# Kernel optimization log

Hardware: AMD Instinct MI355X
Metric: run time of the kernel (lower is better)

Reference implementation:

```python
import jax, jax.numpy as jnp
import numpy as np
from jax import lax
jax.config.update('jax_enable_x64', True)

SR = 44100
BLOCK = 512
N_MELS = 80
N_ALLPASS = 256
N_HARM = 512
N_NOISE = 256
HID = 256
B = 16
NF = 400
T = NF * BLOCK
N_OUT = N_ALLPASS + N_HARM + N_NOISE


def upsample(sig, factor):
    # torch: interpolate(cat(sig, sig[-1:]), size=n*factor+1, mode='linear', align_corners=True)[:-1]
    b, n, c = sig.shape
    ext = jnp.concatenate([sig, sig[:, -1:]], axis=1)  # (b, n+1, c)
    w = (jnp.arange(factor, dtype=jnp.float32) / factor)[None, None, :, None]
    up = ext[:, :-1, None, :] * (1.0 - w) + ext[:, 1:, None, :] * w
    return up.reshape(b, n * factor, c)


def hann_periodic(n):
    return 0.5 - 0.5 * jnp.cos(2.0 * np.pi * jnp.arange(n, dtype=jnp.float32) / n)


def freq_impulse_response(mag, hann_window, half_width=None):
    # mag: (b, nf, m) complex -> ir: (b, nf, 2*(m-1)) in causal (rolled) form
    ir = jnp.fft.irfft(mag).astype(jnp.float32)
    n = ir.shape[-1]
    if hann_window:
        if half_width is None:
            w = jnp.roll(hann_periodic(n), n // 2)
            ir = jnp.roll(ir * w, n // 2, axis=-1)
        else:
            # dynamic hann window with per-frame half width (b, nf, 1)
            w = jnp.arange(-(n // 2), (n + 1) // 2, dtype=jnp.float32) / half_width
            w = jnp.where(w > 1.0, 0.0, w)
            w = (1.0 + jnp.cos(np.pi * w)) * 0.5
            ir = jnp.roll(ir, n // 2, axis=-1) * w
    else:
        ir = jnp.roll(ir, n // 2, axis=-1)
    return ir


def fft_convolve(audio, ir):
    b, t = audio.shape
    nf, ir_size = ir.shape[1], ir.shape[2]
    hop = t // nf
    frame = 2 * hop
    fft_size = frame + ir_size - 1
    chunks = jnp.pad(audio, ((0, 0), (hop, hop))).reshape(b, nf + 2, hop)
    frames = jnp.concatenate([chunks[:, :-1], chunks[:, 1:]], axis=-1)  # (b, nf+1, frame)
    bart = 1.0 - jnp.abs(2.0 * jnp.arange(frame, dtype=jnp.float32) / frame - 1.0)
    frames = frames * bart
    ir_ext = jnp.concatenate([ir, ir[:, -1:]], axis=1)  # repeat last IR frame
    out_f = jnp.fft.irfft(jnp.fft.rfft(frames, fft_size) * jnp.fft.rfft(ir_ext, fft_size), fft_size).astype(jnp.float32)
    n_out = nf + 1
    length = (n_out - 1) * hop + fft_size
    idx = (jnp.arange(n_out)[:, None] * hop + jnp.arange(fft_size)[None, :]).reshape(-1)
    out = jnp.zeros((b, length), jnp.float32).at[:, idx].add(out_f.reshape(b, -1))
    return out[:, hop:t + hop]


def conv1d_same(x, w, bias):
    y = lax.conv_general_dilated(x, w, (1,), [(1, 1)], dimension_numbers=('NCH', 'OIH', 'NCH'))
    return y + bias[None, :, None]


def mel2ctrl(mel, phase, conv1_w, conv1_b, gn_g, gn_b, conv2_w, conv2_b, phase_w, phase_b, ln_g, ln_b, out_w, out_b):
    h = conv1d_same(mel.transpose(0, 2, 1), conv1_w, conv1_b)  # (b, 256, nf)
    b, c, l = h.shape
    g = h.reshape(b, 4, c // 4, l)  # GroupNorm(4, 256)
    mu = g.mean((2, 3), keepdims=True)
    var = g.var((2, 3), keepdims=True)
    h = ((g - mu) / jnp.sqrt(var + 1e-5)).reshape(b, c, l)
    h = h * gn_g[None, :, None] + gn_b[None, :, None]
    h = jnp.where(h >= 0, h, 0.01 * h)  # LeakyReLU
    h = conv1d_same(h, conv2_w, conv2_b).transpose(0, 2, 1)  # (b, nf, 256)
    pe = jnp.concatenate([jnp.sin(phase), jnp.cos(phase)], axis=-1) @ phase_w.T + phase_b
    h = h + pe
    mu = h.mean(-1, keepdims=True)
    var = h.var(-1, keepdims=True)
    h = (h - mu) / jnp.sqrt(var + 1e-5) * ln_g + ln_b
    out = h @ out_w.T + out_b
    gd = out[..., :N_ALLPASS]
    hm = out[..., N_ALLPASS:N_ALLPASS + N_HARM]
    nm = out[..., N_ALLPASS + N_HARM:]
    return gd, hm, nm


def setup_inputs():
    key = jax.random.key(0)
    ks = jax.random.split(key, 8)
    s = 0.02
    return {
        'mel_frames': jax.random.normal(ks[0], (B, NF, N_MELS), jnp.float32),
        'f0_frames': jax.random.uniform(ks[1], (B, NF, 1), jnp.float32) * 400.0 + 100.0,
        'initial_phase': jnp.zeros((B, 1, 1), jnp.float32),
        'uniform_noise': jax.random.uniform(ks[2], (B, T), jnp.float32),
        'conv1_w': jax.random.normal(ks[3], (HID, N_MELS, 3), jnp.float32) * s,
        'conv1_b': jnp.zeros((HID,), jnp.float32),
        'gn_g': jnp.ones((HID,), jnp.float32),
        'gn_b': jnp.zeros((HID,), jnp.float32),
        'conv2_w': jax.random.normal(ks[4], (HID, HID, 3), jnp.float32) * s,
        'conv2_b': jnp.zeros((HID,), jnp.float32),
        'phase_w': jax.random.normal(ks[5], (HID, 2), jnp.float32) * s,
        'phase_b': jnp.zeros((HID,), jnp.float32),
        'ln_g': jnp.ones((HID,), jnp.float32),
        'ln_b': jnp.zeros((HID,), jnp.float32),
        'out_w': jax.random.normal(ks[6], (N_OUT, HID), jnp.float32) * s,
        'out_b': jnp.zeros((N_OUT,), jnp.float32),
    }


def reference(mel_frames, f0_frames, initial_phase, uniform_noise, conv1_w, conv1_b, gn_g, gn_b, conv2_w, conv2_b, phase_w, phase_b, ln_g, ln_b, out_w, out_b):
    f0 = upsample(f0_frames, BLOCK)  # (B, T, 1)
    # double-precision wrapped phase accumulation
    x = jnp.cumsum(f0.astype(jnp.float64) / SR, axis=1) + initial_phase.astype(jnp.float64) / (2.0 * np.pi)
    x = (x - jnp.round(x)).astype(jnp.float32)
    phase_frames = 2.0 * np.pi * x[:, ::BLOCK, :]  # (B, NF, 1)
    gd_raw, hm_raw, nm_raw = mel2ctrl(mel_frames, phase_frames, conv1_w, conv1_b, gn_g, gn_b, conv2_w, conv2_b, phase_w, phase_b, ln_g, ln_b, out_w, out_b)
    group_delay = np.pi * jnp.tanh(gd_raw)
    src_param = jnp.exp(hm_raw)
    noise_param = jnp.exp(nm_raw) / 128.0
    combtooth = jnp.sinc(SR * x / (f0 + 0.001))[..., 0]  # (B, T)
    allpass = jnp.exp(1j * jnp.cumsum(group_delay, axis=-1).astype(jnp.complex64))
    harmonic = fft_convolve(combtooth, freq_impulse_response(allpass, hann_window=False))
    half_width = 1.5 * SR / (f0_frames + 0.001)  # (B, NF, 1)
    harmonic = fft_convolve(harmonic, freq_impulse_response(src_param.astype(jnp.complex64), True, half_width))
    noise = uniform_noise * 2.0 - 1.0
    noise = fft_convolve(noise, freq_impulse_response(noise_param.astype(jnp.complex64), True, None))
    signal = harmonic + noise
    return signal, phase_frames, harmonic, noise
```

## Files before the change

### kernel.cpp

```cpp
#include <hip/hip_runtime.h>
#include <math.h>

#define BATCH 16
#define NF_ 400
#define TLEN 204800
#define NMELS 80
#define HID 256
#define SRD 44100.0

static constexpr size_t S_ = 1638400;
static constexpr size_t OFF_COMB = 0;
static constexpr size_t OFF_H1   = 2 * S_;
static constexpr size_t OFF_H2   = 3 * S_;
static constexpr size_t OFF_IR1  = 2 * S_;
static constexpr size_t OFF_PHI  = 4 * S_;
static constexpr size_t OFF_NSP  = 5 * S_;
static constexpr size_t OFF_HTMP = 4 * S_;
static constexpr size_t OFF_SRC  = 6 * S_;
static constexpr size_t OFF_IR3  = 6 * S_;
static constexpr size_t OFF_IR2  = 8 * S_;
static constexpr size_t OFF_FSUM = 12 * S_;
static constexpr size_t OFF_PREF = 12 * S_ + 12800;
static constexpr size_t OFF_GN   = 12 * S_ + 25600;

__device__ __forceinline__ float cs7_f0_at(const float* f0f, int b, int n, int k) {
    float a = f0f[b * NF_ + n];
    float c = f0f[b * NF_ + min(n + 1, NF_ - 1)];
    float w = (float)k * (1.0f / 512.0f);
    return __fadd_rn(__fmul_rn(a, 1.0f - w), __fmul_rn(c, w));
}

__global__ void cs7_fsum(const float* __restrict__ f0f, double* __restrict__ fsum) {
    int gid = blockIdx.x * blockDim.x + threadIdx.x;
    if (gid >= BATCH * NF_) return;
    int b = gid / NF_, n = gid % NF_;
    double s = 0.0;
    for (int k = 0; k < 512; ++k) s += (double)cs7_f0_at(f0f, b, n, k) / SRD;
    fsum[gid] = s;
}

__global__ void cs7_prefix(const double* __restrict__ fsum, double* __restrict__ pref) {
    int b = threadIdx.x;
    if (b >= BATCH) return;
    double run = 0.0;
    for (int n = 0; n < NF_; ++n) { pref[b * NF_ + n] = run; run += fsum[b * NF_ + n]; }
}

__global__ __launch_bounds__(512) void cs7_phase(const float* __restrict__ f0f,
        const float* __restrict__ ip, const double* __restrict__ pref,
        float* __restrict__ comb, float* __restrict__ phase_out) {
    __shared__ double sc[512];
    int b = blockIdx.x / NF_, n = blockIdx.x % NF_;
    int k = threadIdx.x;
    float f0 = cs7_f0_at(f0f, b, n, k);
    sc[k] = (double)f0 / SRD;
    __syncthreads();
    for (int off = 1; off < 512; off <<= 1) {
        double v = (k >= off) ? sc[k - off] : 0.0;
        __syncthreads();
        sc[k] += v;
        __syncthreads();
    }
    double xd = pref[b * NF_ + n] + sc[k] + (double)ip[b] / (2.0 * M_PI);
    xd -= rint(xd);
    float xf = (float)xd;
    double zd = 44100.0 * (double)xf / ((double)f0 + 0.001);
    double pz = M_PI * zd;
    comb[(size_t)b * TLEN + n * 512 + k] = (zd == 0.0) ? 1.0f : (float)(sin(pz) / pz);
    if (k == 0) phase_out[b * NF_ + n] = (float)(2.0 * M_PI * (double)xf);
}

__global__ __launch_bounds__(256) void cs7_conv1x3(const float* __restrict__ mel,
        const float* __restrict__ w1, const float* __restrict__ b1, float* __restrict__ h1) {
    __shared__ float m3[3][NMELS];
    int b = blockIdx.x / NF_, l = blockIdx.x % NF_;
    int tid = threadIdx.x;
    for (int i = tid; i < 3 * NMELS; i += 256) {
        int tap = i / NMELS, ic = i % NMELS;
        int li = l + tap - 1;
        m3[tap][ic] = (li >= 0 && li < NF_) ? mel[((size_t)b * NF_ + li) * NMELS + ic] : 0.0f;
    }
    __syncthreads();
    int oc = tid;
    double acc = (double)b1[oc];
    const float* wp = w1 + (size_t)oc * NMELS * 3;
    for (int ic = 0; ic < NMELS; ++ic)
        acc += (double)m3[0][ic] * (double)wp[ic * 3]
             + (double)m3[1][ic] * (double)wp[ic * 3 + 1]
             + (double)m3[2][ic] * (double)wp[ic * 3 + 2];
    h1[((size_t)b * NF_ + l) * HID + oc] = (float)acc;
}

__global__ __launch_bounds__(256) void cs7_gnstats(const float* __restrict__ h1, float* __restrict__ gn) {
    __shared__ double rs[256], rq[256];
    int b = blockIdx.x >> 2, g = blockIdx.x & 3;
    int tid = threadIdx.x;
    double s = 0.0, q = 0.0;
    for (int i = tid; i < 64 * NF_; i += 256) {
        int l = i >> 6, c = g * 64 + (i & 63);
        float v = h1[((size_t)b * NF_ + l) * HID + c];
        s += v; q += (double)v * v;
    }
    rs[tid] = s; rq[tid] = q;
    __syncthreads();
    for (int off = 128; off > 0; off >>= 1) {
        if (tid < off) { rs[tid] += rs[tid + off]; rq[tid] += rq[tid + off]; }
        __syncthreads();
    }
    if (tid == 0) {
        double mu = rs[0] / (64.0 * NF_);
        double var = rq[0] / (64.0 * NF_) - mu * mu;
        gn[blockIdx.x * 2] = (float)mu;
        gn[blockIdx.x * 2 + 1] = (float)(1.0 / sqrt(var + 1e-5));
    }
}

__global__ __launch_bounds__(256) void cs7_conv2ln(const float* __restrict__ h1,
        const float* __restrict__ gn, const float* __restrict__ gng, const float* __restrict__ gnb,
        const float* __restrict__ w2, const float* __restrict__ b2,
        const float* __restrict__ pw, const float* __restrict__ pb,
        const float* __restrict__ lng, const float* __restrict__ lnb,
        const float* __restrict__ phase, float* __restrict__ h2) {
    __shared__ float cols[10][HID];
    __shared__ double rsum[256], rsq[256];
    int b = blockIdx.x / 50, l0 = (blockIdx.x % 50) * 8;
    int tid = threadIdx.x;
    for (int i = tid; i < 10 * HID; i += 256) {
        int lc = i >> 8, c = i & 255;
        int l = l0 + lc - 1;
        float v = 0.0f;
        if (l >= 0 && l < NF_) {
            float hv = h1[((size_t)b * NF_ + l) * HID + c];
            int g = c >> 6;
            double vv = ((double)hv - (double)gn[(b * 4 + g) * 2]) * (double)gn[(b * 4 + g) * 2 + 1]
                        * (double)gng[c] + (double)gnb[c];
            v = (float)(vv >= 0.0 ? vv : 0.01 * vv);
        }
        cols[lc][c] = v;
    }
    __syncthreads();
    int oc = tid;
    double acc[8];
    #pragma unroll
    for (int lt = 0; lt < 8; ++lt) acc[lt] = (double)b2[oc];
    const float* wp = w2 + (size_t)oc * HID * 3;
    for (int ic = 0; ic < HID; ++ic) {
        double w0 = (double)wp[ic * 3], w1v = (double)wp[ic * 3 + 1], w2v = (double)wp[ic * 3 + 2];
        float cc[10];
        #pragma unroll
        for (int j = 0; j < 10; ++j) cc[j] = cols[j][ic];
        #pragma unroll
        for (int lt = 0; lt < 8; ++lt)
            acc[lt] += (double)cc[lt] * w0 + (double)cc[lt + 1] * w1v + (double)cc[lt + 2] * w2v;
    }
    for (int lt = 0; lt < 8; ++lt) {
        int l = l0 + lt;
        double ph = (double)phase[b * NF_ + l];
        double sp, cp; sincos(ph, &sp, &cp);
        double v = acc[lt] + sp * (double)pw[oc * 2] + cp * (double)pw[oc * 2 + 1] + (double)pb[oc];
        rsum[tid] = v; rsq[tid] = v * v;
        __syncthreads();
        for (int off = 128; off > 0; off >>= 1) {
            if (tid < off) { rsum[tid] += rsum[tid + off]; rsq[tid] += rsq[tid + off]; }
            __syncthreads();
        }
        double mu = rsum[0] * (1.0 / 256.0);
        double var = rsq[0] * (1.0 / 256.0) - mu * mu;
        double rstd = 1.0 / sqrt(var + 1e-5);
        __syncthreads();
        h2[((size_t)b * NF_ + l) * HID + oc] = (float)((v - mu) * rstd * (double)lng[oc] + (double)lnb[oc]);
    }
}

__global__ __launch_bounds__(256) void cs7_proj(const float* __restrict__ h2,
        const float* __restrict__ ow, const float* __restrict__ ob,
        float* __restrict__ phi, float* __restrict__ srcspec, float* __restrict__ nspec) {
    __shared__ float hrow[8][HID];
    __shared__ double ssc[256];
    int b = blockIdx.x / 50, l0 = (blockIdx.x % 50) * 8;
    int tid = threadIdx.x;
    for (int i = tid; i < 8 * HID; i += 256) {
        int lc = i >> 8, c = i & 255;
        hrow[lc][c] = h2[((size_t)b * NF_ + l0 + lc) * HID + c];
    }
    __syncthreads();
    double a0[8], a1[8], a2[8], a3[8];
    #pragma unroll
    for (int lt = 0; lt < 8; ++lt) {
        a0[lt] = (double)ob[tid];       a1[lt] = (double)ob[256 + tid];
        a2[lt] = (double)ob[512 + tid]; a3[lt] = (double)ob[768 + tid];
    }
    const float* w0p = ow + (size_t)tid * HID;
    const float* w1p = ow + (size_t)(256 + tid) * HID;
    const float* w2p = ow + (size_t)(512 + tid) * HID;
    const float* w3p = ow + (size_t)(768 + tid) * HID;
    for (int ic = 0; ic < HID; ++ic) {
        double w0 = (double)w0p[ic], w1v = (double)w1p[ic], w2v = (double)w2p[ic], w3v = (double)w3p[ic];
        #pragma unroll
        for (int lt = 0; lt < 8; ++lt) {
            double h = (double)hrow[lt][ic];
            a0[lt] += h * w0; a1[lt] += h * w1v; a2[lt] += h * w2v; a3[lt] += h * w3v;
        }
    }
    for (int lt = 0; lt < 8; ++lt) {
        size_t bl = (size_t)b * NF_ + (l0 + lt);
        double gdv = M_PI * tanh(a0[lt]);
        ssc[tid] = gdv;
        __syncthreads();
        for (int off = 1; off < 256; off <<= 1) {
            double v = (tid >= off) ? ssc[tid - off] : 0.0;
            __syncthreads();
            ssc[tid] += v;
            __syncthreads();
        }
        phi[bl * 256 + tid] = (float)ssc[tid];
        __syncthreads();
        srcspec[bl * 512 + tid] = (float)exp(a1[lt]);
        srcspec[bl * 512 + 256 + tid] = (float)exp(a2[lt]);
        nspec[bl * 256 + tid] = (float)(exp(a3[lt]) * (1.0 / 128.0));
    }
}

__global__ __launch_bounds__(256) void cs7_ir_allpass(const float* __restrict__ phi, float* __restrict__ ir1) {
    __shared__ float cph[256], sph[256];
    size_t bl = blockIdx.x;
    int tid = threadIdx.x;
    {
        float ph = phi[bl * 256 + tid];
        cph[tid] = 2.0f * cosf(ph); sph[tid] = 2.0f * sinf(ph);
    }
    __syncthreads();
    for (int t = tid; t < 510; t += 256) {
        double ang = 2.0 * M_PI * (double)t / 510.0;
        double srd_, crd; sincos(ang, &srd_, &crd);
        double sj, cj;    sincos(16.0 * ang, &sj, &cj);
        float crf = (float)crd, srf = (float)srd_;
        double cD = crd, sD = srd_;
        float acc = 0.5f * (cph[0] + ((t & 1) ? -cph[255] : cph[255]));
        for (int k0 = 1; k0 <= 254; k0 += 16) {
            float c = (float)cD, s = (float)sD;
            int ke = min(k0 + 16, 255);
            for (int k = k0; k < ke; ++k) {
                acc += cph[k] * c - sph[k] * s;
                float cn = c * crf - s * srf;
                float sn = s * crf + c * srf;
                c = cn; s = sn;
            }
            double nc = cD * cj - sD * sj;
            double ns = sD * cj + cD * sj;
            cD = nc; sD = ns;
        }
        int j = t + 255; if (j >= 510) j -= 510;
        ir1[bl * 510 + j] = acc * (1.0f / 510.0f);
    }
}

__device__ __forceinline__ float cs7_hw_win(int j, float hw) {
    float wv = (float)(j - 511) / hw;
    if (wv > 1.0f) wv = 0.0f;
    return (1.0f + cosf((float)M_PI * wv)) * 0.5f;
}

__global__ __launch_bounds__(256) void cs7_ir_src(const float* __restrict__ srcspec,
        const float* __restrict__ f0f, float* __restrict__ ir2) {
    __shared__ float sp[512];
    size_t bl = blockIdx.x;
    int b = blockIdx.x / NF_, l = blockIdx.x % NF_;
    int tid = threadIdx.x;
    sp[tid] = 2.0f * srcspec[bl * 512 + tid];
    sp[tid + 256] = 2.0f * srcspec[bl * 512 + 256 + tid];
    __syncthreads();
    float hw = 66150.0f / (f0f[b * NF_ + l] + 0.001f);
    for (int t = tid; t < 512; t += 256) {
        double ang = 2.0 * M_PI * (double)t / 1022.0;
        double srd_, crd; sincos(ang, &srd_, &crd);
        double sj, cj;    sincos(16.0 * ang, &sj, &cj);
        float crf = (float)crd, srf = (float)srd_;
        double cD = crd, sD = srd_;
        float acc = 0.5f * (sp[0] + ((t & 1) ? -sp[511] : sp[511]));
        for (int k0 = 1; k0 <= 510; k0 += 16) {
            float c = (float)cD, s = (float)sD;
            int ke = min(k0 + 16, 511);
            for (int k = k0; k < ke; ++k) {
                acc += sp[k] * c;
                float cn = c * crf - s * srf;
                float sn = s * crf + c * srf;
                c = cn; s = sn;
            }
            double nc = cD * cj - sD * sj;
            double ns = sD * cj + cD * sj;
            cD = nc; sD = ns;
        }
        float raw = acc * (1.0f / 1022.0f);
        {
            int j = t + 511; if (j >= 1022) j -= 1022;
            ir2[bl * 1022 + j] = raw * cs7_hw_win(j, hw);
        }
        if (t >= 1 && t <= 510) {
            int j = 511 - t;
            ir2[bl * 1022 + j] = raw * cs7_hw_win(j, hw);
        }
    }
}

__global__ __launch_bounds__(256) void cs7_ir_noise(const float* __restrict__ nspec, float* __restrict__ ir3) {
    __shared__ float sp[256];
    size_t bl = blockIdx.x;
    int t = threadIdx.x;
    sp[t] = 2.0f * nspec[bl * 256 + t];
    __syncthreads();
    double ang = 2.0 * M_PI * (double)t / 510.0;
    double srd_, crd; sincos(ang, &srd_, &crd);
    double sj, cj;    sincos(16.0 * ang, &sj, &cj);
    float crf = (float)crd, srf = (float)srd_;
    double cD = crd, sD = srd_;
    float acc = 0.5f * (sp[0] + ((t & 1) ? -sp[255] : sp[255]));
    for (int k0 = 1; k0 <= 254; k0 += 16) {
        float c = (float)cD, s = (float)sD;
        int ke = min(k0 + 16, 255);
        for (int k = k0; k < ke; ++k) {
            acc += sp[k] * c;
            float cn = c * crf - s * srf;
            float sn = s * crf + c * srf;
            c = cn; s = sn;
        }
        double nc = cD * cj - sD * sj;
        double ns = sD * cj + cD * sj;
        cD = nc; sD = ns;
    }
    float raw = acc * (1.0f / 510.0f);
    {
        int j = t + 255; if (j >= 510) j -= 510;
        float win = 0.5f - 0.5f * cosf((float)(2.0 * M_PI) * (float)j / 510.0f);
        ir3[bl * 510 + j] = raw * win;
    }
    if (t >= 1 && t <= 254) {
        int j = 255 - t;
        float win = 0.5f - 0.5f * cosf((float)(2.0 * M_PI) * (float)j / 510.0f);
        ir3[bl * 510 + j] = raw * win;
    }
}

template<int IRS, int NFRM, int MOFF>
__global__ __launch_bounds__(256) void cs7_conv(const float* __restrict__ audio,
        const float* __restrict__ ir, float* __restrict__ out, float scale, float shift) {
    constexpr int PAD = 264;
    constexpr int W   = (IRS + 2 * PAD + 3) & ~3;
    constexpr int FRW = 1040;
    __shared__ float4 sir4[NFRM][W / 4];
    __shared__ float4 fr4[NFRM][FRW / 4];
    float* sir = (float*)sir4;
    float* frp = (float*)fr4;
    int b = blockIdx.x / 200, q = blockIdx.x % 200;
    int t0 = q * 1024;
    int m_lo = 2 * q + MOFF;
    int tid = threadIdx.x;

    for (int i = tid; i < NFRM * FRW; i += 256) {
        int fi = i / FRW, kk = i - fi * FRW;
        int k = kk - 6;
        float sv = 0.0f;
        if (k >= 0 && k < 1024) {
            int m = m_lo + fi;
            int idx = (m << 9) + k - 512;
            float v = 0.0f;
            if (m >= 0 && m <= 400 && idx >= 0 && idx < TLEN)
                v = audio[(size_t)b * TLEN + idx] * scale + shift;
            float bart = 1.0f - fabsf((float)k * (1.0f / 512.0f) - 1.0f);
            sv = v * bart;
        }
        frp[fi * FRW + kk] = sv;
    }
    for (int i = tid; i < NFRM * W; i += 256) {
        int fi = i / W, x = i - fi * W;
        int j = (IRS - 1 + PAD) - x;
        int m = m_lo + fi;
        float v = 0.0f;
        if (j >= 0 && j < IRS && m >= 0 && m <= 400)
            v = ir[((size_t)b * NF_ + min(m, 399)) * IRS + j];
        sir[fi * W + x] = v;
    }
    __syncthreads();

    int tb = t0 + tid * 4;
    int wtid0 = tid & ~63;
    float acc0 = 0, acc1 = 0, acc2 = 0, acc3 = 0;
    #pragma unroll
    for (int fi = 0; fi < NFRM; ++fi) {
        int m = m_lo + fi;
        if (m < 0 || m > 400) continue;
        int d0w = t0 + wtid0 * 4 + 512 - (m << 9);
        int klo = max(0, d0w - (IRS - 1));
        int khi = min(1023, d0w + 255);
        if (klo > khi) continue;
        int kc0 = (((klo - 2) & ~3) + 2);
        int nch = ((khi - kc0) >> 2) + 1;
        int d0  = t0 + tid * 4 + 512 - (m << 9);
        const float4* sp = (const float4*)(sir + fi * W + ((IRS + PAD - 4) - d0 + kc0));
        const float4* fp = (const float4*)(frp + fi * FRW + 6 + kc0);
        float4 A = sp[0];
        for (int c = 0; c < nch; ++c) {
            float4 B = sp[c + 1];
            float4 F = fp[c];
            acc3 += F.x * A.x; acc2 += F.x * A.y; acc1 += F.x * A.z; acc0 += F.x * A.w;
            acc3 += F.y * A.y; acc2 += F.y * A.z; acc1 += F.y * A.w; acc0 += F.y * B.x;
            acc3 += F.z * A.z; acc2 += F.z * A.w; acc1 += F.z * B.x; acc0 += F.z * B.y;
            acc3 += F.w * A.w; acc2 += F.w * B.x; acc1 += F.w * B.y; acc0 += F.w * B.z;
            A = B;
        }
    }
    *(float4*)(out + (size_t)b * TLEN + tb) = make_float4(acc0, acc1, acc2, acc3);
}

__global__ void cs7_add(const float* __restrict__ a, const float* __restrict__ b,
                        float* __restrict__ o, int n4) {
    int i = blockIdx.x * blockDim.x + threadIdx.x;
    if (i < n4) {
        float4 x = ((const float4*)a)[i];
        float4 y = ((const float4*)b)[i];
        ((float4*)o)[i] = make_float4(x.x + y.x, x.y + y.y, x.z + y.z, x.w + y.w);
    }
}

extern "C" void kernel_launch(void* const* d_in, const int* in_sizes, int n_in,
                              void* d_out, int out_size, void* d_ws, size_t ws_size,
                              hipStream_t stream) {
    const float* mel   = (const float*)d_in[0];
    const float* f0f   = (const float*)d_in[1];
    const float* ip    = (const float*)d_in[2];
    const float* unoi  = (const float*)d_in[3];
    const float* w1    = (const float*)d_in[4];
    const float* b1    = (const float*)d_in[5];
    const float* gng   = (const float*)d_in[6];
    const float* gnb   = (const float*)d_in[7];
    const float* w2    = (const float*)d_in[8];
    const float* b2    = (const float*)d_in[9];
    const float* pw    = (const float*)d_in[10];
    const float* pb    = (const float*)d_in[11];
    const float* lng   = (const float*)d_in[12];
    const float* lnb   = (const float*)d_in[13];
    const float* ow    = (const float*)d_in[14];
    const float* ob    = (const float*)d_in[15];
    float* out = (float*)d_out;
    float* ws  = (float*)d_ws;

    float*  comb = ws + OFF_COMB;
    float*  h1   = ws + OFF_H1;
    float*  h2   = ws + OFF_H2;
    float*  ir1  = ws + OFF_IR1;
    float*  phi  = ws + OFF_PHI;
    float*  nsp  = ws + OFF_NSP;
    float*  htmp = ws + OFF_HTMP;
    float*  ssp  = ws + OFF_SRC;
    float*  ir3  = ws + OFF_IR3;
    float*  ir2  = ws + OFF_IR2;
    double* fsum = (double*)(ws + OFF_FSUM);
    double* pref = (double*)(ws + OFF_PREF);
    float*  gn   = ws + OFF_GN;

    float* out_sig   = out;
    float* out_phase = out + (size_t)BATCH * TLEN;
    float* out_harm  = out_phase + BATCH * NF_;
    float* out_noise = out_harm + (size_t)BATCH * TLEN;

    cs7_fsum<<<25, 256, 0, stream>>>(f0f, fsum);
    cs7_prefix<<<1, 16, 0, stream>>>(fsum, pref);
    cs7_phase<<<BATCH * NF_, 512, 0, stream>>>(f0f, ip, pref, comb, out_phase);
    cs7_conv1x3<<<BATCH * NF_, 256, 0, stream>>>(mel, w1, b1, h1);
    cs7_gnstats<<<64, 256, 0, stream>>>(h1, gn);
    cs7_conv2ln<<<BATCH * 50, 256, 0, stream>>>(h1, gn, gng, gnb, w2, b2, pw, pb, lng, lnb, out_phase, h2);
    cs7_proj<<<BATCH * 50, 256, 0, stream>>>(h2, ow, ob, phi, ssp, nsp);
    cs7_ir_allpass<<<BATCH * NF_, 256, 0, stream>>>(phi, ir1);
    cs7_ir_src<<<BATCH * NF_, 256, 0, stream>>>(ssp, f0f, ir2);
    cs7_ir_noise<<<BATCH * NF_, 256, 0, stream>>>(nsp, ir3);
    cs7_conv<510, 4, -1><<<BATCH * 200, 256, 0, stream>>>(comb, ir1, htmp, 1.0f, 0.0f);
    cs7_conv<1022, 5, -2><<<BATCH * 200, 256, 0, stream>>>(htmp, ir2, out_harm, 1.0f, 0.0f);
    cs7_conv<510, 4, -1><<<BATCH * 200, 256, 0, stream>>>(unoi, ir3, out_noise, 2.0f, -1.0f);
    cs7_add<<<(BATCH * TLEN / 4 + 255) / 256, 256, 0, stream>>>(out_harm, out_noise, out_sig, BATCH * TLEN / 4);
}
```

Baseline: 2.853 ms.

## Pre-window frames in global memory and widen direct-conv tiles to 8 outputs per thread

Producers now write Bartlett-windowed overlapping frames straight into a frame buffer. The phase kernel and the first harmonic convolution each write their output split into two crossfade halves, and a staging kernel does the same for noise. The convolution kernel reads those frames from global memory instead of rebuilding them in LDS. Each thread now computes 8 outputs instead of 4 over a 2048-sample tile, using a swizzled LDS IR row and a 3-way unrolled register rotation, which cuts LDS traffic per FMA. This costs extra memsets, a staging pass, more workspace and per-thread registers, and frames are re-read from global/L2 instead of shared memory.

```diff
diff --git a/kernel.cpp b/kernel.cpp
--- a/kernel.cpp
+++ b/kernel.cpp
@@ -8,51 +8,47 @@
 #define HID 256
 #define SRD 44100.0
 
-static constexpr size_t S_ = 1638400;
-static constexpr size_t OFF_COMB = 0;
-static constexpr size_t OFF_H1   = 2 * S_;
-static constexpr size_t OFF_H2   = 3 * S_;
-static constexpr size_t OFF_IR1  = 2 * S_;
-static constexpr size_t OFF_PHI  = 4 * S_;
-static constexpr size_t OFF_NSP  = 5 * S_;
-static constexpr size_t OFF_HTMP = 4 * S_;
-static constexpr size_t OFF_SRC  = 6 * S_;
-static constexpr size_t OFF_IR3  = 6 * S_;
-static constexpr size_t OFF_IR2  = 8 * S_;
-static constexpr size_t OFF_FSUM = 12 * S_;
-static constexpr size_t OFF_PREF = 12 * S_ + 12800;
-static constexpr size_t OFF_GN   = 12 * S_ + 25600;
-
-__device__ __forceinline__ float cs7_f0_at(const float* f0f, int b, int n, int k) {
+static constexpr size_t S_   = 1638400;
+static constexpr size_t FRSZ = (size_t)6416 * 1028;
+static constexpr size_t OFF_A    = 0;
+static constexpr size_t OFF_JN   = FRSZ;
+static constexpr size_t OFF_SSP  = 2 * FRSZ;
+static constexpr size_t OFF_IR1  = OFF_SSP + 2 * S_;
+static constexpr size_t OFF_IR3  = OFF_IR1 + 3264000;
+static constexpr size_t OFF_FSUM = OFF_IR3 + 3264000;
+static constexpr size_t OFF_PREF = OFF_FSUM + 12800;
+static constexpr size_t OFF_GN   = OFF_PREF + 12800;
+
+__device__ __forceinline__ float cs8_f0_at(const float* f0f, int b, int n, int k) {
     float a = f0f[b * NF_ + n];
     float c = f0f[b * NF_ + min(n + 1, NF_ - 1)];
     float w = (float)k * (1.0f / 512.0f);
     return __fadd_rn(__fmul_rn(a, 1.0f - w), __fmul_rn(c, w));
 }
 
-__global__ void cs7_fsum(const float* __restrict__ f0f, double* __restrict__ fsum) {
+__global__ void cs8_fsum(const float* __restrict__ f0f, double* __restrict__ fsum) {
     int gid = blockIdx.x * blockDim.x + threadIdx.x;
     if (gid >= BATCH * NF_) return;
     int b = gid / NF_, n = gid % NF_;
     double s = 0.0;
-    for (int k = 0; k < 512; ++k) s += (double)cs7_f0_at(f0f, b, n, k) / SRD;
+    for (int k = 0; k < 512; ++k) s += (double)cs8_f0_at(f0f, b, n, k) / SRD;
     fsum[gid] = s;
 }
 
-__global__ void cs7_prefix(const double* __restrict__ fsum, double* __restrict__ pref) {
+__global__ void cs8_prefix(const double* __restrict__ fsum, double* __restrict__ pref) {
     int b = threadIdx.x;
     if (b >= BATCH) return;
     double run = 0.0;
     for (int n = 0; n < NF_; ++n) { pref[b * NF_ + n] = run; run += fsum[b * NF_ + n]; }
 }
 
-__global__ __launch_bounds__(512) void cs7_phase(const float* __restrict__ f0f,
+__global__ __launch_bounds__(512) void cs8_phase(const float* __restrict__ f0f,
         const float* __restrict__ ip, const double* __restrict__ pref,
-        float* __restrict__ comb, float* __restrict__ phase_out) {
+        float* __restrict__ frA, float* __restrict__ phase_out) {
     __shared__ double sc[512];
     int b = blockIdx.x / NF_, n = blockIdx.x % NF_;
     int k = threadIdx.x;
-    float f0 = cs7_f0_at(f0f, b, n, k);
+    float f0 = cs8_f0_at(f0f, b, n, k);
     sc[k] = (double)f0 / SRD;
     __syncthreads();
     for (int off = 1; off < 512; off <<= 1) {
@@ -66,11 +62,15 @@
     float xf = (float)xd;
     double zd = 44100.0 * (double)xf / ((double)f0 + 0.001);
     double pz = M_PI * zd;
-    comb[(size_t)b * TLEN + n * 512 + k] = (zd == 0.0) ? 1.0f : (float)(sin(pz) / pz);
+    float cv = (zd == 0.0) ? 1.0f : (float)(sin(pz) / pz);
+    float wb = (float)k * (1.0f / 512.0f);
+    size_t row = (size_t)(b * 401 + n) * 1028;
+    frA[row + 512 + k]  = cv * (1.0f - wb);
+    frA[row + 1028 + k] = cv * wb;
     if (k == 0) phase_out[b * NF_ + n] = (float)(2.0 * M_PI * (double)xf);
 }
 
-__global__ __launch_bounds__(256) void cs7_conv1x3(const float* __restrict__ mel,
+__global__ __launch_bounds__(256) void cs8_conv1x3(const float* __restrict__ mel,
         const float* __restrict__ w1, const float* __restrict__ b1, float* __restrict__ h1) {
     __shared__ float m3[3][NMELS];
     int b = blockIdx.x / NF_, l = blockIdx.x % NF_;
@@ -91,7 +91,7 @@
     h1[((size_t)b * NF_ + l) * HID + oc] = (float)acc;
 }
 
-__global__ __launch_bounds__(256) void cs7_gnstats(const float* __restrict__ h1, float* __restrict__ gn) {
+__global__ __launch_bounds__(256) void cs8_gnstats(const float* __restrict__ h1, float* __restrict__ gn) {
     __shared__ double rs[256], rq[256];
     int b = blockIdx.x >> 2, g = blockIdx.x & 3;
     int tid = threadIdx.x;
@@ -115,7 +115,7 @@
     }
 }
 
-__global__ __launch_bounds__(256) void cs7_conv2ln(const float* __restrict__ h1,
+__global__ __launch_bounds__(256) void cs8_conv2ln(const float* __restrict__ h1,
         const float* __restrict__ gn, const float* __restrict__ gng, const float* __restrict__ gnb,
         const float* __restrict__ w2, const float* __restrict__ b2,
         const float* __restrict__ pw, const float* __restrict__ pb,
@@ -172,7 +172,7 @@
     }
 }
 
-__global__ __launch_bounds__(256) void cs7_proj(const float* __restrict__ h2,
+__global__ __launch_bounds__(256) void cs8_proj(const float* __restrict__ h2,
         const float* __restrict__ ow, const float* __restrict__ ob,
         float* __restrict__ phi, float* __restrict__ srcspec, float* __restrict__ nspec) {
     __shared__ float hrow[8][HID];
@@ -221,7 +221,7 @@
     }
 }
 
-__global__ __launch_bounds__(256) void cs7_ir_allpass(const float* __restrict__ phi, float* __restrict__ ir1) {
+__global__ __launch_bounds__(256) void cs8_ir_allpass(const float* __restrict__ phi, float* __restrict__ ir1) {
     __shared__ float cph[256], sph[256];
     size_t bl = blockIdx.x;
     int tid = threadIdx.x;
@@ -255,13 +255,13 @@
     }
 }
 
-__device__ __forceinline__ float cs7_hw_win(int j, float hw) {
+__device__ __forceinline__ float cs8_hw_win(int j, float hw) {
     float wv = (float)(j - 511) / hw;
     if (wv > 1.0f) wv = 0.0f;
     return (1.0f + cosf((float)M_PI * wv)) * 0.5f;
 }
 
-__global__ __launch_bounds__(256) void cs7_ir_src(const float* __restrict__ srcspec,
+__global__ __launch_bounds__(256) void cs8_ir_src(const float* __restrict__ srcspec,
         const float* __restrict__ f0f, float* __restrict__ ir2) {
     __shared__ float sp[512];
     size_t bl = blockIdx.x;
@@ -294,16 +294,16 @@
         float raw = acc * (1.0f / 1022.0f);
         {
             int j = t + 511; if (j >= 1022) j -= 1022;
-            ir2[bl * 1022 + j] = raw * cs7_hw_win(j, hw);
+            ir2[bl * 1022 + j] = raw * cs8_hw_win(j, hw);
         }
         if (t >= 1 && t <= 510) {
             int j = 511 - t;
-            ir2[bl * 1022 + j] = raw * cs7_hw_win(j, hw);
-        }
-    }
-}
-
-__global__ __launch_bounds__(256) void cs7_ir_noise(const float* __restrict__ nspec, float* __restrict__ ir3) {
+            ir2[bl * 1022 + j] = raw * cs8_hw_win(j, hw);
+        }
+    }
+}
+
+__global__ __launch_bounds__(256) void cs8_ir_noise(const float* __restrict__ nspec, float* __restrict__ ir3) {
     __shared__ float sp[256];
     size_t bl = blockIdx.x;
     int t = threadIdx.x;
@@ -341,78 +341,120 @@
     }
 }
 
-template<int IRS, int NFRM, int MOFF>
-__global__ __launch_bounds__(256) void cs7_conv(const float* __restrict__ audio,
-        const float* __restrict__ ir, float* __restrict__ out, float scale, float shift) {
-    constexpr int PAD = 264;
-    constexpr int W   = (IRS + 2 * PAD + 3) & ~3;
-    constexpr int FRW = 1040;
-    __shared__ float4 sir4[NFRM][W / 4];
-    __shared__ float4 fr4[NFRM][FRW / 4];
-    float* sir = (float*)sir4;
-    float* frp = (float*)fr4;
-    int b = blockIdx.x / 200, q = blockIdx.x % 200;
-    int t0 = q * 1024;
-    int m_lo = 2 * q + MOFF;
-    int tid = threadIdx.x;
-
-    for (int i = tid; i < NFRM * FRW; i += 256) {
-        int fi = i / FRW, kk = i - fi * FRW;
-        int k = kk - 6;
-        float sv = 0.0f;
-        if (k >= 0 && k < 1024) {
-            int m = m_lo + fi;
-            int idx = (m << 9) + k - 512;
-            float v = 0.0f;
-            if (m >= 0 && m <= 400 && idx >= 0 && idx < TLEN)
-                v = audio[(size_t)b * TLEN + idx] * scale + shift;
-            float bart = 1.0f - fabsf((float)k * (1.0f / 512.0f) - 1.0f);
-            sv = v * bart;
-        }
-        frp[fi * FRW + kk] = sv;
-    }
+__global__ __launch_bounds__(256) void cs8_stagef(const float* __restrict__ audio,
+        float* __restrict__ frw, float scale, float shift) {
+    int bm = blockIdx.x;
+    int b = bm / 401, m = bm % 401;
+    int tid = threadIdx.x;
+    for (int kk = tid; kk < 1028; kk += 256) {
+        float v = 0.0f;
+        if (kk < 1024) {
+            int idx = (m << 9) + kk - 512;
+            if (idx >= 0 && idx < TLEN) {
+                float a = audio[(size_t)b * TLEN + idx] * scale + shift;
+                float bart = 1.0f - fabsf((float)kk * (1.0f / 512.0f) - 1.0f);
+                v = a * bart;
+            }
+        }
+        frw[(size_t)bm * 1028 + kk] = v;
+    }
+}
+
+__device__ __forceinline__ int cs8_swz(int B) { return B ^ ((B >> 3) & 7); }
+
+__device__ __forceinline__ void cs8_fma8(const float4 F, const float4 A,
+        const float4 B, const float4 C, float acc[8]) {
+    const float w[12] = {A.x,A.y,A.z,A.w,B.x,B.y,B.z,B.w,C.x,C.y,C.z,C.w};
+    #pragma unroll
+    for (int a = 0; a < 8; ++a)
+        acc[a] += F.x * w[8 - a] + F.y * w[9 - a] + F.z * w[10 - a] + F.w * w[11 - a];
+}
+
+template<int IRS, int NFRM, int MOFF, int FOUT>
+__global__ __launch_bounds__(256) void cs8_conv(const float* __restrict__ frw,
+        const float* __restrict__ ir, float* __restrict__ out) {
+    constexpr int PAD = 515;
+    constexpr int R = IRS - 1 + PAD;
+    constexpr int W = (R + 526) & ~3;
+    __shared__ __align__(16) float sir[NFRM][W];
+    int b = blockIdx.x / 100, q = blockIdx.x % 100;
+    int t0 = q * 2048;
+    int m_lo = (t0 >> 9) + MOFF;
+    int tid = threadIdx.x;
+
     for (int i = tid; i < NFRM * W; i += 256) {
         int fi = i / W, x = i - fi * W;
-        int j = (IRS - 1 + PAD) - x;
+        int j = R - x;
         int m = m_lo + fi;
         float v = 0.0f;
         if (j >= 0 && j < IRS && m >= 0 && m <= 400)
             v = ir[((size_t)b * NF_ + min(m, 399)) * IRS + j];
-        sir[fi * W + x] = v;
-    }
-    __syncthreads();
-
-    int tb = t0 + tid * 4;
-    int wtid0 = tid & ~63;
-    float acc0 = 0, acc1 = 0, acc2 = 0, acc3 = 0;
+        int p = (cs8_swz(x >> 2) << 2) | (x & 3);
+        sir[fi][p] = v;
+    }
+    __syncthreads();
+
+    int tb = t0 + tid * 8;
+    int wt0 = tid & ~63;
+    float acc[8] = {0, 0, 0, 0, 0, 0, 0, 0};
     #pragma unroll
     for (int fi = 0; fi < NFRM; ++fi) {
         int m = m_lo + fi;
         if (m < 0 || m > 400) continue;
-        int d0w = t0 + wtid0 * 4 + 512 - (m << 9);
+        int d0w = t0 + wt0 * 8 + 512 - (m << 9);
         int klo = max(0, d0w - (IRS - 1));
-        int khi = min(1023, d0w + 255);
+        int khi = min(1023, d0w + 511);
         if (klo > khi) continue;
-        int kc0 = (((klo - 2) & ~3) + 2);
-        int nch = ((khi - kc0) >> 2) + 1;
-        int d0  = t0 + tid * 4 + 512 - (m << 9);
-        const float4* sp = (const float4*)(sir + fi * W + ((IRS + PAD - 4) - d0 + kc0));
-        const float4* fp = (const float4*)(frp + fi * FRW + 6 + kc0);
-        float4 A = sp[0];
-        for (int c = 0; c < nch; ++c) {
-            float4 B = sp[c + 1];
-            float4 F = fp[c];
-            acc3 += F.x * A.x; acc2 += F.x * A.y; acc1 += F.x * A.z; acc0 += F.x * A.w;
-            acc3 += F.y * A.y; acc2 += F.y * A.z; acc1 += F.y * A.w; acc0 += F.y * B.x;
-            acc3 += F.z * A.z; acc2 += F.z * A.w; acc1 += F.z * B.x; acc0 += F.z * B.y;
-            acc3 += F.w * A.w; acc2 += F.w * B.x; acc1 += F.w * B.y; acc0 += F.w * B.z;
-            A = B;
-        }
-    }
-    *(float4*)(out + (size_t)b * TLEN + tb) = make_float4(acc0, acc1, acc2, acc3);
-}
-
-__global__ void cs7_add(const float* __restrict__ a, const float* __restrict__ b,
+        int kcs = __builtin_amdgcn_readfirstlane(klo & ~3);
+        int nch = ((__builtin_amdgcn_readfirstlane(khi) - kcs) >> 2) + 1;
+        int d0 = t0 + tid * 8 + 512 - (m << 9);
+        int Bb = (R - d0 + kcs - 8) >> 2;
+        const float4* row4 = (const float4*)&sir[fi][0];
+        const float4* fp4 = (const float4*)(frw + (size_t)(b * 401 + m) * 1028 + kcs);
+        float4 r0 = row4[cs8_swz(Bb)];
+        float4 r1 = row4[cs8_swz(Bb + 1)];
+        float4 r2;
+        int c = 0;
+        for (; c + 3 <= nch; c += 3) {
+            float4 F0 = fp4[c];
+            r2 = row4[cs8_swz(Bb + c + 2)];
+            cs8_fma8(F0, r0, r1, r2, acc);
+            float4 F1 = fp4[c + 1];
+            r0 = row4[cs8_swz(Bb + c + 3)];
+            cs8_fma8(F1, r1, r2, r0, acc);
+            float4 F2 = fp4[c + 2];
+            r1 = row4[cs8_swz(Bb + c + 4)];
+            cs8_fma8(F2, r2, r0, r1, acc);
+        }
+        for (; c < nch; ++c) {
+            float4 F = fp4[c];
+            r2 = row4[cs8_swz(Bb + c + 2)];
+            cs8_fma8(F, r0, r1, r2, acc);
+            r0 = r1; r1 = r2;
+        }
+    }
+    if (FOUT == 0) {
+        float* o = out + (size_t)b * TLEN + tb;
+        *(float4*)o = make_float4(acc[0], acc[1], acc[2], acc[3]);
+        *(float4*)(o + 4) = make_float4(acc[4], acc[5], acc[6], acc[7]);
+    } else {
+        int km = tb & 511;
+        int m1 = tb >> 9;
+        float* r1p = out + (size_t)(b * 401 + m1) * 1028;
+        float bw[8];
+        #pragma unroll
+        for (int j2 = 0; j2 < 8; ++j2) bw[j2] = (float)(km + j2) * (1.0f / 512.0f);
+        *(float4*)(r1p + 512 + km) = make_float4(acc[0] * (1.f - bw[0]), acc[1] * (1.f - bw[1]),
+                                                 acc[2] * (1.f - bw[2]), acc[3] * (1.f - bw[3]));
+        *(float4*)(r1p + 512 + km + 4) = make_float4(acc[4] * (1.f - bw[4]), acc[5] * (1.f - bw[5]),
+                                                     acc[6] * (1.f - bw[6]), acc[7] * (1.f - bw[7]));
+        float* r2p = r1p + 1028;
+        *(float4*)(r2p + km) = make_float4(acc[0] * bw[0], acc[1] * bw[1], acc[2] * bw[2], acc[3] * bw[3]);
+        *(float4*)(r2p + km + 4) = make_float4(acc[4] * bw[4], acc[5] * bw[5], acc[6] * bw[6], acc[7] * bw[7]);
+    }
+}
+
+__global__ void cs8_add(const float* __restrict__ a, const float* __restrict__ b,
                         float* __restrict__ o, int n4) {
     int i = blockIdx.x * blockDim.x + threadIdx.x;
     if (i < n4) {
@@ -444,16 +486,16 @@
     float* out = (float*)d_out;
     float* ws  = (float*)d_ws;
 
-    float*  comb = ws + OFF_COMB;
-    float*  h1   = ws + OFF_H1;
-    float*  h2   = ws + OFF_H2;
+    float*  frA  = ws + OFF_A;
+    float*  frJ  = ws + OFF_JN;
+    float*  h1   = ws + OFF_JN;
+    float*  h2   = ws + OFF_JN + S_;
+    float*  phi  = ws + OFF_JN + 2 * S_;
+    float*  nsp  = ws + OFF_JN + 3 * S_;
+    float*  ssp  = ws + OFF_SSP;
     float*  ir1  = ws + OFF_IR1;
-    float*  phi  = ws + OFF_PHI;
-    float*  nsp  = ws + OFF_NSP;
-    float*  htmp = ws + OFF_HTMP;
-    float*  ssp  = ws + OFF_SRC;
     float*  ir3  = ws + OFF_IR3;
-    float*  ir2  = ws + OFF_IR2;
+    float*  ir2  = ws + OFF_A;
     double* fsum = (double*)(ws + OFF_FSUM);
     double* pref = (double*)(ws + OFF_PREF);
     float*  gn   = ws + OFF_GN;
@@ -463,18 +505,21 @@
     float* out_harm  = out_phase + BATCH * NF_;
     float* out_noise = out_harm + (size_t)BATCH * TLEN;
 
-    cs7_fsum<<<25, 256, 0, stream>>>(f0f, fsum);
-    cs7_prefix<<<1, 16, 0, stream>>>(fsum, pref);
-    cs7_phase<<<BATCH * NF_, 512, 0, stream>>>(f0f, ip, pref, comb, out_phase);
-    cs7_conv1x3<<<BATCH * NF_, 256, 0, stream>>>(mel, w1, b1, h1);
-    cs7_gnstats<<<64, 256, 0, stream>>>(h1, gn);
-    cs7_conv2ln<<<BATCH * 50, 256, 0, stream>>>(h1, gn, gng, gnb, w2, b2, pw, pb, lng, lnb, out_phase, h2);
-    cs7_proj<<<BATCH * 50, 256, 0, stream>>>(h2, ow, ob, phi, ssp, nsp);
-    cs7_ir_allpass<<<BATCH * NF_, 256, 0, stream>>>(phi, ir1);
-    cs7_ir_src<<<BATCH * NF_, 256, 0, stream>>>(ssp, f0f, ir2);
-    cs7_ir_noise<<<BATCH * NF_, 256, 0, stream>>>(nsp, ir3);
-    cs7_conv<510, 4, -1><<<BATCH * 200, 256, 0, stream>>>(comb, ir1, htmp, 1.0f, 0.0f);
-    cs7_conv<1022, 5, -2><<<BATCH * 200, 256, 0, stream>>>(htmp, ir2, out_harm, 1.0f, 0.0f);
-    cs7_conv<510, 4, -1><<<BATCH * 200, 256, 0, stream>>>(unoi, ir3, out_noise, 2.0f, -1.0f);
-    cs7_add<<<(BATCH * TLEN / 4 + 255) / 256, 256, 0, stream>>>(out_harm, out_noise, out_sig, BATCH * TLEN / 4);
-}
+    hipMemsetAsync(frA, 0, FRSZ * sizeof(float), stream);
+    cs8_fsum<<<25, 256, 0, stream>>>(f0f, fsum);
+    cs8_prefix<<<1, 16, 0, stream>>>(fsum, pref);
+    cs8_phase<<<BATCH * NF_, 512, 0, stream>>>(f0f, ip, pref, frA, out_phase);
+    cs8_conv1x3<<<BATCH * NF_, 256, 0, stream>>>(mel, w1, b1, h1);
+    cs8_gnstats<<<64, 256, 0, stream>>>(h1, gn);
+    cs8_conv2ln<<<BATCH * 50, 256, 0, stream>>>(h1, gn, gng, gnb, w2, b2, pw, pb, lng, lnb, out_phase, h2);
+    cs8_proj<<<BATCH * 50, 256, 0, stream>>>(h2, ow, ob, phi, ssp, nsp);
+    cs8_ir_allpass<<<BATCH * NF_, 256, 0, stream>>>(phi, ir1);
+    cs8_ir_noise<<<BATCH * NF_, 256, 0, stream>>>(nsp, ir3);
+    cs8_stagef<<<BATCH * 401, 256, 0, stream>>>(unoi, frJ, 2.0f, -1.0f);
+    cs8_conv<510, 6, -1, 0><<<BATCH * 100, 256, 0, stream>>>(frJ, ir3, out_noise);
+    hipMemsetAsync(frJ, 0, FRSZ * sizeof(float), stream);
+    cs8_conv<510, 6, -1, 1><<<BATCH * 100, 256, 0, stream>>>(frA, ir1, frJ);
+    cs8_ir_src<<<BATCH * NF_, 256, 0, stream>>>(ssp, f0f, ir2);
+    cs8_conv<1022, 7, -2, 0><<<BATCH * 100, 256, 0, stream>>>(frJ, ir2, out_harm);
+    cs8_add<<<(BATCH * TLEN / 4 + 255) / 256, 256, 0, stream>>>(out_harm, out_noise, out_sig, BATCH * TLEN / 4);
+}
```

Result: no change. 2.819 ms (-1.2%).
